# Performance work log

Measured on AMD Instinct MI355X. Metric: run time of the kernel, lower is better.

## Reference

```python
import jax, jax.numpy as jnp
import numpy as np

NBINS = (128, 64, 32)
N_POINTS = 250_000
N_GENES = 5000
N_GENES_OI = 500
SUM_H = sum(NBINS)            # 224
SUM_W = sum(n - 1 for n in NBINS)  # 221


def _calculate_widths(unnormalized_widths):
    return jax.nn.softmax(unnormalized_widths, axis=-1)


def _calculate_bin_locations(widths):
    bl = jnp.cumsum(widths, axis=-1)
    bl = bl.at[..., -1].set(1.0)
    pad = [(0, 0)] * (bl.ndim - 1) + [(1, 0)]
    return jnp.pad(bl, pad)


def _calculate_heights(unnormalized_heights, widths):
    e = jnp.exp(unnormalized_heights)
    # trapezoid-rule area so pdf integrates to 1
    area = jnp.sum(0.5 * (e[..., :-1] + e[..., 1:]) * widths, axis=-1, keepdims=True)
    return e / area


def _calculate_bin_left_cdf(heights, widths):
    cdf = jnp.cumsum(0.5 * (heights[..., :-1] + heights[..., 1:]) * widths, axis=-1)
    cdf = cdf.at[..., -1].set(1.0)
    pad = [(0, 0)] * (cdf.ndim - 1) + [(1, 0)]
    return jnp.pad(cdf, pad)


def _quadratic_spline(x, widths, heights, bin_left_cdf, bin_locations):
    # all per-point: widths [N,nb], heights [N,nb+1], cdf/locations [N,nb+1]
    nb = widths.shape[-1]
    bin_idx = jnp.clip(jnp.sum(x[:, None] >= bin_locations, axis=-1) - 1, 0, nb - 1)

    def take(a, i):
        return jnp.take_along_axis(a, i[:, None], axis=-1)[:, 0]

    in_bl = take(bin_locations, bin_idx)
    in_cdf = take(bin_left_cdf, bin_idx)
    h_left = take(heights, bin_idx)
    h_right = take(heights, bin_idx + 1)
    w = take(widths, bin_idx)

    a = 0.5 * (h_right - h_left) * w
    b = h_left * w
    alpha = (x - in_bl) / w
    out = a * alpha * alpha + b * alpha + in_cdf
    logabsdet = jnp.log(alpha * (h_right - h_left) + h_left)
    return jnp.clip(out, 0.0, 1.0), logabsdet


def setup_inputs() -> dict:
    key = jax.random.key(0)
    k1, k2, k3, k4, k5, k6 = jax.random.split(key, 6)
    return {
        "x": jax.random.uniform(k1, (N_POINTS,), dtype=jnp.float32),
        "delta": jax.random.normal(k2, (N_POINTS, SUM_H), dtype=jnp.float32),
        "heights_weight": jax.random.normal(k3, (N_GENES, SUM_H), dtype=jnp.float32),
        "widths_weight": jax.random.normal(k4, (N_GENES, SUM_W), dtype=jnp.float32),
        "genes_oi": jax.random.randint(k5, (N_GENES_OI,), 0, N_GENES, dtype=jnp.int32),
        "local_gene_ix": jax.random.randint(k6, (N_POINTS,), 0, N_GENES_OI, dtype=jnp.int32),
    }


def reference(x, delta, heights_weight, widths_weight, genes_oi, local_gene_ix):
    # sparse embedding gather for the genes in the minibatch
    uh_all = heights_weight[genes_oi]   # [G_oi, sum_h]
    uw_all = widths_weight[genes_oi]    # [G_oi, sum_w]

    outputs = x
    logabsdet = jnp.zeros_like(x)
    h_off = 0
    w_off = 0
    d_off = 0
    for n in NBINS:
        uw = uw_all[:, w_off:w_off + (n - 1)]          # [G_oi, n-1]
        uh = uh_all[:, h_off:h_off + n]                # [G_oi, n]
        dh = delta[:, d_off:d_off + n]                 # [N, n]

        widths_g = _calculate_widths(uw)               # [G_oi, n-1]
        bin_loc_g = _calculate_bin_locations(widths_g) # [G_oi, n]

        widths = widths_g[local_gene_ix]               # [N, n-1]
        bin_locations = bin_loc_g[local_gene_ix]       # [N, n]
        uh_p = uh[local_gene_ix] + dh                  # [N, n]
        heights = _calculate_heights(uh_p, widths)     # [N, n]
        bin_left_cdf = _calculate_bin_left_cdf(heights, widths)  # [N, n]

        outputs, lad = _quadratic_spline(outputs, widths, heights, bin_left_cdf, bin_locations)
        logabsdet = logabsdet + lad

        h_off += n
        w_off += n - 1
        d_off += n
    return outputs, logabsdet
```

## Files before the change

### kernel.cpp

```cpp
#include <hip/hip_runtime.h>
#include <math.h>

#define SUM_H 224
#define SUM_W 221
#define ROWP  224

typedef float f32x4 __attribute__((ext_vector_type(4)));
typedef float f32x2 __attribute__((ext_vector_type(2)));

__global__ __launch_bounds__(64) void gene_tables_kernel(
    const float* __restrict__ widths_weight,
    const int*   __restrict__ genes_oi,
    float* __restrict__ bl_t,
    int n_genes)
{
    int g = blockIdx.x;
    if (g >= n_genes) return;
    int gi = genes_oi[g];
    int l  = threadIdx.x;

    const float* wsrc  = widths_weight + (size_t)gi * SUM_W;
    float*       bldst = bl_t + (size_t)g * ROWP;

    const int ns[3]   = {128, 64, 32};
    const int woff[3] = {0, 127, 190};
    const int toff[3] = {0, 128, 192};

    for (int lev = 0; lev < 3; lev++) {
        int m  = ns[lev] - 1;
        int j0 = 2 * l, j1 = 2 * l + 1;
        float u0 = (j0 < m) ? wsrc[woff[lev] + j0] : -1e30f;
        float u1 = (j1 < m) ? wsrc[woff[lev] + j1] : -1e30f;
        float mx = fmaxf(u0, u1);
        #pragma unroll
        for (int msk = 32; msk >= 1; msk >>= 1)
            mx = fmaxf(mx, __shfl_xor(mx, msk, 64));
        float e0 = (j0 < m) ? __expf(u0 - mx) : 0.f;
        float e1 = (j1 < m) ? __expf(u1 - mx) : 0.f;
        float local = e0 + e1;
        float incl  = local;
        #pragma unroll
        for (int off = 1; off < 64; off <<= 1) {
            float t = __shfl_up(incl, off, 64);
            if (l >= off) incl += t;
        }
        float total = __shfl(incl, 63, 64);
        float inv   = 1.0f / total;
        float excl  = incl - local;
        float c0 = (excl + e0) * inv;
        float c1 = (excl + e0 + e1) * inv;
        if (j0 <= m - 2) bldst[toff[lev] + j0 + 1] = c0;
        if (j1 <= m - 2) bldst[toff[lev] + j1 + 1] = c1;
        if (l == 0) {
            bldst[toff[lev]]     = 0.0f;
            bldst[toff[lev] + m] = 1.0f;
        }
    }
}

template<int CTRL>
__device__ __forceinline__ float dppf(float v) {
    return __builtin_bit_cast(float,
        __builtin_amdgcn_update_dpp(0, __builtin_bit_cast(int, v), CTRL, 0xF, 0xF, true));
}
template<int CTRL>
__device__ __forceinline__ int dppi(int v) {
    return __builtin_amdgcn_update_dpp(0, v, CTRL, 0xF, 0xF, true);
}
__device__ __forceinline__ float row16_sum(float v) {
    v += dppf<0x121>(v);
    v += dppf<0x122>(v);
    v += dppf<0x124>(v);
    v += dppf<0x128>(v);
    return v;
}
__device__ __forceinline__ int row16_sum_i(int v) {
    v += dppi<0x121>(v);
    v += dppi<0x122>(v);
    v += dppi<0x124>(v);
    v += dppi<0x128>(v);
    return v;
}

template<int K>
struct Lvl {
    float E[K + 1];
    float bl[K];
    float s[K];
    float bln;
    float inva;
    float larea;
};

template<int K>
__device__ __forceinline__ void lvl_fetch(const float* __restrict__ dh,
                                          const float* __restrict__ uh,
                                          const float* __restrict__ blp,
                                          int e, Lvl<K>& L)
{
    const int j = K * e;
    if constexpr (K == 8) {
        *(f32x4*)&L.E[0]  = *(const f32x4*)(uh  + j);
        *(f32x4*)&L.E[4]  = *(const f32x4*)(uh  + j + 4);
        *(f32x4*)&L.s[0]  = __builtin_nontemporal_load((const f32x4*)(dh + j));
        *(f32x4*)&L.s[4]  = __builtin_nontemporal_load((const f32x4*)(dh + j + 4));
        *(f32x4*)&L.bl[0] = *(const f32x4*)(blp + j);
        *(f32x4*)&L.bl[4] = *(const f32x4*)(blp + j + 4);
    } else if constexpr (K == 4) {
        *(f32x4*)&L.E[0]  = *(const f32x4*)(uh  + j);
        *(f32x4*)&L.s[0]  = __builtin_nontemporal_load((const f32x4*)(dh + j));
        *(f32x4*)&L.bl[0] = *(const f32x4*)(blp + j);
    } else {
        *(f32x2*)&L.E[0]  = *(const f32x2*)(uh  + j);
        *(f32x2*)&L.s[0]  = __builtin_nontemporal_load((const f32x2*)(dh + j));
        *(f32x2*)&L.bl[0] = *(const f32x2*)(blp + j);
    }
}

template<int K>
__device__ __forceinline__ void lvl_finish(int e, Lvl<K>& L)
{
    L.bln = __shfl_down(L.bl[0], 1, 16);
    #pragma unroll
    for (int k = 0; k < K; k++) L.E[k] = __expf(L.E[k] + L.s[k]);
    L.E[K] = __shfl_down(L.E[0], 1, 16);
    #pragma unroll
    for (int k = 0; k < K - 1; k++)
        L.s[k] = (L.E[k] + L.E[k + 1]) * (0.5f * (L.bl[k + 1] - L.bl[k]));
    {
        float sl = (L.E[K - 1] + L.E[K]) * (0.5f * (L.bln - L.bl[K - 1]));
        L.s[K - 1] = (e == 15) ? 0.f : sl;
    }
    float a = 0.f;
    #pragma unroll
    for (int k = 0; k < K; k++) a += L.s[k];
    a = row16_sum(a);
    L.inva  = __builtin_amdgcn_rcpf(a);
    L.larea = __logf(a);
}

template<int N, int K>
__device__ __forceinline__ void lvl_apply(const Lvl<K>& L, int e, float& x, float& lad)
{
    constexpr int LOGK = (K == 8) ? 3 : (K == 4) ? 2 : 1;

    int   cnt  = (x >= L.bl[0]) ? 1 : 0;
    float part = 0.f;
    float El = L.E[0], Er = L.E[1], inb = L.bl[0], blr = L.bl[1];
    #pragma unroll
    for (int k = 1; k < K; k++) {
        bool pk = (x >= L.bl[k]);
        cnt  += pk ? 1 : 0;
        part += pk ? L.s[k - 1] : 0.f;
        bool sel = pk && ((k < K - 1) || (e != 15));
        float cr = (k == K - 1) ? L.bln : L.bl[k + 1];
        El  = sel ? L.E[k]     : El;
        Er  = sel ? L.E[k + 1] : Er;
        inb = sel ? L.bl[k]    : inb;
        blr = sel ? cr         : blr;
    }
    part += (x >= L.bln) ? L.s[K - 1] : 0.f;

    cnt  = row16_sum_i(cnt);
    part = row16_sum(part);

    int idx = cnt - 1;
    if (idx > N - 2) idx = N - 2;
    const int owner = idx >> LOGK;

    El  = __shfl(El,  owner, 16);
    Er  = __shfl(Er,  owner, 16);
    inb = __shfl(inb, owner, 16);
    blr = __shfl(blr, owner, 16);

    float w     = blr - inb;
    float dE    = Er - El;
    float alpha = (x - inb) * __builtin_amdgcn_rcpf(w);
    float poly  = fmaf(fmaf(0.5f * w * dE, alpha, El * w), alpha, part);
    float outv  = poly * L.inva;
    lad += __logf(fmaf(alpha, dE, El)) - L.larea;
    x = __builtin_amdgcn_fmed3f(outv, 0.0f, 1.0f);
}

__global__ __launch_bounds__(256, 4) void spline_kernel(
    const float* __restrict__ x_in,
    const float* __restrict__ delta,
    const int*   __restrict__ lgx,
    const int*   __restrict__ genes_oi,
    const float* __restrict__ heights_weight,
    const float* __restrict__ bl_t,
    float* __restrict__ out,
    float* __restrict__ lad_out,
    int n_points)
{
    int tid = blockIdx.x * blockDim.x + threadIdx.x;
    int p = tid >> 4;
    int e = tid & 15;
    if (p >= n_points) return;

    int g  = lgx[p];
    int gi = genes_oi[g];
    const float* dh = delta          + (size_t)p  * SUM_H;
    const float* uh = heights_weight + (size_t)gi * SUM_H;
    const float* bl = bl_t + (size_t)g * ROWP;

    Lvl<8> L0; Lvl<4> L1; Lvl<2> L2;
    lvl_fetch<8>(dh,       uh,       bl,       e, L0);
    lvl_fetch<4>(dh + 128, uh + 128, bl + 128, e, L1);
    lvl_fetch<2>(dh + 192, uh + 192, bl + 192, e, L2);
    float x   = x_in[p];
    float lad = 0.f;

    lvl_finish<8>(e, L0);
    lvl_finish<4>(e, L1);
    lvl_apply<128, 8>(L0, e, x, lad);
    lvl_finish<2>(e, L2);
    lvl_apply<64,  4>(L1, e, x, lad);
    lvl_apply<32,  2>(L2, e, x, lad);

    if (e == 0) {
        out[p]     = x;
        lad_out[p] = lad;
    }
}

extern "C" void kernel_launch(void* const* d_in, const int* in_sizes, int n_in,
                              void* d_out, int out_size, void* d_ws, size_t ws_size,
                              hipStream_t stream)
{
    const float* x        = (const float*)d_in[0];
    const float* delta    = (const float*)d_in[1];
    const float* hw       = (const float*)d_in[2];
    const float* ww       = (const float*)d_in[3];
    const int*   genes_oi = (const int*)  d_in[4];
    const int*   lgx      = (const int*)  d_in[5];

    int n_points   = in_sizes[0];
    int n_genes_oi = in_sizes[4];

    float* bl_t = (float*)d_ws;

    hipLaunchKernelGGL(gene_tables_kernel, dim3(n_genes_oi), dim3(64), 0, stream,
                       ww, genes_oi, bl_t, n_genes_oi);

    const int threads = 256;
    const int ppb     = threads / 16;
    const int blocks  = (n_points + ppb - 1) / ppb;
    hipLaunchKernelGGL(spline_kernel, dim3(blocks), dim3(threads), 0, stream,
                       x, delta, lgx, genes_oi, hw, bl_t,
                       (float*)d_out, (float*)d_out + n_points, n_points);
}
```

Measured before the change: 332.7 us.

## Pack per-gene heights into table and process two points per 16-lane group

The gene-table kernel now also copies each selected gene's height weights into a combined per-gene row, so the spline kernel no longer does the genes_oi indirection or reads heights_weight directly. Each 16-lane group now handles two points with interleaved finish/apply stages, which raises memory-level parallelism and latency hiding, and x, gene index and output accesses are vectorised. Bin ownership is found with a wave ballot plus popcount instead of a DPP integer reduction. In exchange, register pressure roughly doubles and the occupancy hint drops from 4 to 3 blocks.

```diff
diff --git a/kernel.cpp b/kernel.cpp
--- a/kernel.cpp
+++ b/kernel.cpp
@@ -3,15 +3,16 @@
 
 #define SUM_H 224
 #define SUM_W 221
-#define ROWP  224
+#define TROW  448
 
 typedef float f32x4 __attribute__((ext_vector_type(4)));
 typedef float f32x2 __attribute__((ext_vector_type(2)));
 
 __global__ __launch_bounds__(64) void gene_tables_kernel(
     const float* __restrict__ widths_weight,
+    const float* __restrict__ heights_weight,
     const int*   __restrict__ genes_oi,
-    float* __restrict__ bl_t,
+    float* __restrict__ tab,
     int n_genes)
 {
     int g = blockIdx.x;
@@ -19,8 +20,11 @@
     int gi = genes_oi[g];
     int l  = threadIdx.x;
 
-    const float* wsrc  = widths_weight + (size_t)gi * SUM_W;
-    float*       bldst = bl_t + (size_t)g * ROWP;
+    const float* wsrc = widths_weight  + (size_t)gi * SUM_W;
+    const float* hsrc = heights_weight + (size_t)gi * SUM_H;
+    float*       trow = tab + (size_t)g * TROW;
+
+    if (l < 56) ((f32x4*)(trow + 224))[l] = ((const f32x4*)hsrc)[l];
 
     const int ns[3]   = {128, 64, 32};
     const int woff[3] = {0, 127, 190};
@@ -49,11 +53,11 @@
         float excl  = incl - local;
         float c0 = (excl + e0) * inv;
         float c1 = (excl + e0 + e1) * inv;
-        if (j0 <= m - 2) bldst[toff[lev] + j0 + 1] = c0;
-        if (j1 <= m - 2) bldst[toff[lev] + j1 + 1] = c1;
+        if (j0 <= m - 2) trow[toff[lev] + j0 + 1] = c0;
+        if (j1 <= m - 2) trow[toff[lev] + j1 + 1] = c1;
         if (l == 0) {
-            bldst[toff[lev]]     = 0.0f;
-            bldst[toff[lev] + m] = 1.0f;
+            trow[toff[lev]]     = 0.0f;
+            trow[toff[lev] + m] = 1.0f;
         }
     }
 }
@@ -62,23 +66,12 @@
 __device__ __forceinline__ float dppf(float v) {
     return __builtin_bit_cast(float,
         __builtin_amdgcn_update_dpp(0, __builtin_bit_cast(int, v), CTRL, 0xF, 0xF, true));
-}
-template<int CTRL>
-__device__ __forceinline__ int dppi(int v) {
-    return __builtin_amdgcn_update_dpp(0, v, CTRL, 0xF, 0xF, true);
 }
 __device__ __forceinline__ float row16_sum(float v) {
     v += dppf<0x121>(v);
     v += dppf<0x122>(v);
     v += dppf<0x124>(v);
     v += dppf<0x128>(v);
-    return v;
-}
-__device__ __forceinline__ int row16_sum_i(int v) {
-    v += dppi<0x121>(v);
-    v += dppi<0x122>(v);
-    v += dppi<0x124>(v);
-    v += dppi<0x128>(v);
     return v;
 }
 
@@ -93,27 +86,36 @@
 };
 
 template<int K>
-__device__ __forceinline__ void lvl_fetch(const float* __restrict__ dh,
-                                          const float* __restrict__ uh,
-                                          const float* __restrict__ blp,
-                                          int e, Lvl<K>& L)
+__device__ __forceinline__ void fetch_delta(const float* __restrict__ dh, int e, Lvl<K>& L)
 {
     const int j = K * e;
     if constexpr (K == 8) {
-        *(f32x4*)&L.E[0]  = *(const f32x4*)(uh  + j);
-        *(f32x4*)&L.E[4]  = *(const f32x4*)(uh  + j + 4);
-        *(f32x4*)&L.s[0]  = __builtin_nontemporal_load((const f32x4*)(dh + j));
-        *(f32x4*)&L.s[4]  = __builtin_nontemporal_load((const f32x4*)(dh + j + 4));
-        *(f32x4*)&L.bl[0] = *(const f32x4*)(blp + j);
-        *(f32x4*)&L.bl[4] = *(const f32x4*)(blp + j + 4);
+        *(f32x4*)&L.s[0] = __builtin_nontemporal_load((const f32x4*)(dh + j));
+        *(f32x4*)&L.s[4] = __builtin_nontemporal_load((const f32x4*)(dh + j + 4));
     } else if constexpr (K == 4) {
-        *(f32x4*)&L.E[0]  = *(const f32x4*)(uh  + j);
-        *(f32x4*)&L.s[0]  = __builtin_nontemporal_load((const f32x4*)(dh + j));
-        *(f32x4*)&L.bl[0] = *(const f32x4*)(blp + j);
+        *(f32x4*)&L.s[0] = __builtin_nontemporal_load((const f32x4*)(dh + j));
     } else {
-        *(f32x2*)&L.E[0]  = *(const f32x2*)(uh  + j);
-        *(f32x2*)&L.s[0]  = __builtin_nontemporal_load((const f32x2*)(dh + j));
-        *(f32x2*)&L.bl[0] = *(const f32x2*)(blp + j);
+        *(f32x2*)&L.s[0] = __builtin_nontemporal_load((const f32x2*)(dh + j));
+    }
+}
+
+template<int K>
+__device__ __forceinline__ void fetch_tab(const float* __restrict__ bl,
+                                          const float* __restrict__ uh,
+                                          int e, Lvl<K>& L)
+{
+    const int j = K * e;
+    if constexpr (K == 8) {
+        *(f32x4*)&L.E[0]  = *(const f32x4*)(uh + j);
+        *(f32x4*)&L.E[4]  = *(const f32x4*)(uh + j + 4);
+        *(f32x4*)&L.bl[0] = *(const f32x4*)(bl + j);
+        *(f32x4*)&L.bl[4] = *(const f32x4*)(bl + j + 4);
+    } else if constexpr (K == 4) {
+        *(f32x4*)&L.E[0]  = *(const f32x4*)(uh + j);
+        *(f32x4*)&L.bl[0] = *(const f32x4*)(bl + j);
+    } else {
+        *(f32x2*)&L.E[0]  = *(const f32x2*)(uh + j);
+        *(f32x2*)&L.bl[0] = *(const f32x2*)(bl + j);
     }
 }
 
@@ -140,17 +142,15 @@
 }
 
 template<int N, int K>
-__device__ __forceinline__ void lvl_apply(const Lvl<K>& L, int e, float& x, float& lad)
-{
-    constexpr int LOGK = (K == 8) ? 3 : (K == 4) ? 2 : 1;
-
-    int   cnt  = (x >= L.bl[0]) ? 1 : 0;
+__device__ __forceinline__ void lvl_apply(const Lvl<K>& L, int e,
+                                          unsigned long long gmask,
+                                          float& x, float& lad)
+{
     float part = 0.f;
     float El = L.E[0], Er = L.E[1], inb = L.bl[0], blr = L.bl[1];
     #pragma unroll
     for (int k = 1; k < K; k++) {
         bool pk = (x >= L.bl[k]);
-        cnt  += pk ? 1 : 0;
         part += pk ? L.s[k - 1] : 0.f;
         bool sel = pk && ((k < K - 1) || (e != 15));
         float cr = (k == K - 1) ? L.bln : L.bl[k + 1];
@@ -161,12 +161,9 @@
     }
     part += (x >= L.bln) ? L.s[K - 1] : 0.f;
 
-    cnt  = row16_sum_i(cnt);
     part = row16_sum(part);
-
-    int idx = cnt - 1;
-    if (idx > N - 2) idx = N - 2;
-    const int owner = idx >> LOGK;
+    unsigned long long b = __ballot(x >= L.bl[0]);
+    int owner = (int)__popcll(b & gmask) - 1;
 
     El  = __shfl(El,  owner, 16);
     Er  = __shfl(Er,  owner, 16);
@@ -182,45 +179,77 @@
     x = __builtin_amdgcn_fmed3f(outv, 0.0f, 1.0f);
 }
 
-__global__ __launch_bounds__(256, 4) void spline_kernel(
+__global__ __launch_bounds__(256, 3) void spline_kernel(
     const float* __restrict__ x_in,
     const float* __restrict__ delta,
     const int*   __restrict__ lgx,
-    const int*   __restrict__ genes_oi,
-    const float* __restrict__ heights_weight,
-    const float* __restrict__ bl_t,
+    const float* __restrict__ tab,
     float* __restrict__ out,
     float* __restrict__ lad_out,
     int n_points)
 {
     int tid = blockIdx.x * blockDim.x + threadIdx.x;
-    int p = tid >> 4;
-    int e = tid & 15;
-    if (p >= n_points) return;
-
-    int g  = lgx[p];
-    int gi = genes_oi[g];
-    const float* dh = delta          + (size_t)p  * SUM_H;
-    const float* uh = heights_weight + (size_t)gi * SUM_H;
-    const float* bl = bl_t + (size_t)g * ROWP;
-
-    Lvl<8> L0; Lvl<4> L1; Lvl<2> L2;
-    lvl_fetch<8>(dh,       uh,       bl,       e, L0);
-    lvl_fetch<4>(dh + 128, uh + 128, bl + 128, e, L1);
-    lvl_fetch<2>(dh + 192, uh + 192, bl + 192, e, L2);
-    float x   = x_in[p];
-    float lad = 0.f;
-
-    lvl_finish<8>(e, L0);
-    lvl_finish<4>(e, L1);
-    lvl_apply<128, 8>(L0, e, x, lad);
-    lvl_finish<2>(e, L2);
-    lvl_apply<64,  4>(L1, e, x, lad);
-    lvl_apply<32,  2>(L2, e, x, lad);
+    int grp = tid >> 4;
+    int e   = tid & 15;
+    int p0  = grp * 2;
+    if (p0 >= n_points) return;
+    bool has1 = (p0 + 1 < n_points);
+
+    int g0, g1;
+    float x0, x1;
+    if (has1) {
+        int2   gg = *(const int2*)  (lgx  + p0);
+        float2 xx = *(const float2*)(x_in + p0);
+        g0 = gg.x; g1 = gg.y; x0 = xx.x; x1 = xx.y;
+    } else {
+        g0 = lgx[p0]; g1 = g0; x0 = x_in[p0]; x1 = x0;
+    }
+
+    const float* dh0 = delta + (size_t)p0 * SUM_H;
+    const float* dh1 = dh0 + SUM_H;
+
+    Lvl<8> A0, B0; Lvl<4> A1, B1; Lvl<2> A2, B2;
+
+    fetch_delta<8>(dh0,       e, A0);
+    fetch_delta<8>(dh1,       e, B0);
+    fetch_delta<4>(dh0 + 128, e, A1);
+    fetch_delta<4>(dh1 + 128, e, B1);
+    fetch_delta<2>(dh0 + 192, e, A2);
+    fetch_delta<2>(dh1 + 192, e, B2);
+
+    const float* t0 = tab + (size_t)g0 * TROW;
+    const float* t1 = tab + (size_t)g1 * TROW;
+    fetch_tab<8>(t0,       t0 + 224, e, A0);
+    fetch_tab<8>(t1,       t1 + 224, e, B0);
+    fetch_tab<4>(t0 + 128, t0 + 352, e, A1);
+    fetch_tab<4>(t1 + 128, t1 + 352, e, B1);
+    fetch_tab<2>(t0 + 192, t0 + 416, e, A2);
+    fetch_tab<2>(t1 + 192, t1 + 416, e, B2);
+
+    unsigned long long gmask = 0xFFFFull << (threadIdx.x & 48);
+    float lad0 = 0.f, lad1 = 0.f;
+
+    lvl_finish<8>(e, A0);
+    lvl_finish<8>(e, B0);
+    lvl_apply<128, 8>(A0, e, gmask, x0, lad0);
+    lvl_finish<4>(e, A1);
+    lvl_finish<4>(e, B1);
+    lvl_apply<128, 8>(B0, e, gmask, x1, lad1);
+    lvl_apply<64,  4>(A1, e, gmask, x0, lad0);
+    lvl_finish<2>(e, A2);
+    lvl_finish<2>(e, B2);
+    lvl_apply<64,  4>(B1, e, gmask, x1, lad1);
+    lvl_apply<32,  2>(A2, e, gmask, x0, lad0);
+    lvl_apply<32,  2>(B2, e, gmask, x1, lad1);
 
     if (e == 0) {
-        out[p]     = x;
-        lad_out[p] = lad;
+        if (has1) {
+            *(f32x2*)(out     + p0) = (f32x2){x0,   x1};
+            *(f32x2*)(lad_out + p0) = (f32x2){lad0, lad1};
+        } else {
+            out[p0]     = x0;
+            lad_out[p0] = lad0;
+        }
     }
 }
 
@@ -238,15 +267,16 @@
     int n_points   = in_sizes[0];
     int n_genes_oi = in_sizes[4];
 
-    float* bl_t = (float*)d_ws;
+    float* tab = (float*)d_ws;
 
     hipLaunchKernelGGL(gene_tables_kernel, dim3(n_genes_oi), dim3(64), 0, stream,
-                       ww, genes_oi, bl_t, n_genes_oi);
+                       ww, hw, genes_oi, tab, n_genes_oi);
 
     const int threads = 256;
-    const int ppb     = threads / 16;
-    const int blocks  = (n_points + ppb - 1) / ppb;
+    const int gpb     = threads / 16;
+    const int ngrp    = (n_points + 1) / 2;
+    const int blocks  = (ngrp + gpb - 1) / gpb;
     hipLaunchKernelGGL(spline_kernel, dim3(blocks), dim3(threads), 0, stream,
-                       x, delta, lgx, genes_oi, hw, bl_t,
+                       x, delta, lgx, tab,
                        (float*)d_out, (float*)d_out + n_points, n_points);
 }
```

After: 330.3 us. No clear change (-0.7%).
